# Kernel tuning notes

Hardware: AMD Instinct MI355X
Metric: run time of the kernel (lower is better)

## Reference

```python
import jax, jax.numpy as jnp
import numpy as np

HEADS = 8
DIM_HEAD = 64
EPS = 1e-5

def chan_norm(x, g, b):
    # LayerNorm over channel dim (axis=1), biased variance
    mean = jnp.mean(x, axis=1, keepdims=True)
    var = jnp.var(x, axis=1, keepdims=True)
    return (x - mean) / jnp.sqrt(var + EPS) * g + b

def l2norm(x):
    n = jnp.sqrt(jnp.sum(x * x, axis=1, keepdims=True))
    return x / jnp.maximum(n, 1e-12)

def fold_heads(x, b):
    # b (h c) H W -> (b h) c H W
    _, hc, H, W = x.shape
    return x.reshape(b, HEADS, DIM_HEAD, H, W).reshape(b * HEADS, DIM_HEAD, H, W)

def setup_inputs() -> dict:
    key = jax.random.key(0)
    ks = jax.random.split(key, 8)
    dim = 256
    inner = HEADS * DIM_HEAD  # 512
    b, Hq, Wq = 8, 96, 96
    Hc, Wc = 64, 64
    s = 1.0 / np.sqrt(dim)
    return {
        "query_source": jax.random.normal(ks[0], (b, dim, Hq, Wq), jnp.float32),
        "context": jax.random.normal(ks[1], (b, dim, Hc, Wc), jnp.float32),
        "qs_g": jnp.ones((1, dim, 1, 1), jnp.float32),
        "qs_b": jnp.zeros((1, dim, 1, 1), jnp.float32),
        "ctx_g": jnp.ones((1, dim, 1, 1), jnp.float32),
        "ctx_b": jnp.zeros((1, dim, 1, 1), jnp.float32),
        "out_g": jnp.ones((1, dim, 1, 1), jnp.float32),
        "out_b": jnp.zeros((1, dim, 1, 1), jnp.float32),
        "w_q": jax.random.normal(ks[2], (inner, dim), jnp.float32) * s,
        "w_kv": jax.random.normal(ks[3], (2 * inner, dim), jnp.float32) * s,
        "w_out": jax.random.normal(ks[4], (dim, inner), jnp.float32) * (1.0 / np.sqrt(inner)),
        "gamma": jnp.full((1,), 0.5, jnp.float32),
    }

def reference(query_source, context, qs_g, qs_b, ctx_g, ctx_b, out_g, out_b, w_q, w_kv, w_out, gamma):
    b, c, Hq, Wq = query_source.shape
    Hc, Wc = context.shape[2], context.shape[3]
    h_top_k = int(Hc ** 0.5)
    w_top_k = int(Wc ** 0.5)

    ctx = chan_norm(context, ctx_g, ctx_b)
    qs = chan_norm(query_source, qs_g, qs_b)

    kv = jnp.einsum('oc,bchw->bohw', w_kv, ctx)  # 1x1 conv, no bias
    k, v = jnp.split(kv, 2, axis=1)
    q = jnp.einsum('oc,bchw->bohw', w_q, qs)

    q = fold_heads(q, b); k = fold_heads(k, b); v = fold_heads(v, b)
    q = l2norm(q); k = l2norm(k)  # cosine-sim attention

    if h_top_k < Hc or w_top_k < Wc:
        k_abs = jnp.abs(k)
        q_probe = jnp.sum(q, axis=(2, 3))  # (bh, d)
        if h_top_k < Hc:
            score_r = jnp.einsum('bc,bch->bh', q_probe, jnp.sum(k_abs, axis=3))
            top_h = jax.lax.top_k(score_r, h_top_k)[1]  # (bh, kh)
            k = jnp.take_along_axis(k, top_h[:, None, :, None], axis=2)
            v = jnp.take_along_axis(v, top_h[:, None, :, None], axis=2)
        if w_top_k < Wc:
            score_c = jnp.einsum('bc,bcw->bw', q_probe, jnp.sum(k_abs, axis=2))
            top_w = jax.lax.top_k(score_c, w_top_k)[1]  # (bh, kw)
            k = jnp.take_along_axis(k, top_w[:, None, None, :], axis=3)
            v = jnp.take_along_axis(v, top_w[:, None, None, :], axis=3)

    # b d h w -> b (h w) d
    flat = lambda t: t.transpose(0, 2, 3, 1).reshape(t.shape[0], -1, t.shape[1])
    qf, kf, vf = flat(q), flat(k), flat(v)

    sim = jnp.einsum('bid,bjd->bij', qf, kf)
    attn = jax.nn.softmax(sim, axis=-1)
    out = jnp.einsum('bij,bjd->bid', attn, vf)  # (bh, Hq*Wq, d)

    out = out.reshape(b, HEADS, Hq, Wq, DIM_HEAD).transpose(0, 1, 4, 2, 3)
    out = out.reshape(b, HEADS * DIM_HEAD, Hq, Wq)
    out = jnp.einsum('oc,bchw->bohw', w_out, out)
    out = chan_norm(out, out_g, out_b)
    return gamma * out + query_source
```

## Files before the change

kernel.cpp:

```cpp
#include <hip/hip_runtime.h>
#include <math.h>


#define EPSN 1e-5f

typedef __attribute__((ext_vector_type(8))) short bf16x8;
typedef __attribute__((ext_vector_type(4))) float f32x4;

__device__ inline unsigned short f2bf(float f) {
    unsigned u = __float_as_uint(f);
    u += 0x7fff + ((u >> 16) & 1);
    return (unsigned short)(u >> 16);
}
__device__ inline float bf2f(unsigned short h) {
    return __uint_as_float((unsigned)h << 16);
}

#define GL2LDS(g, s) __builtin_amdgcn_global_load_lds( \
    (const __attribute__((address_space(1))) void*)(g), \
    (__attribute__((address_space(3))) void*)(s), 16, 0, 0)

__global__ __launch_bounds__(256) void cvt_split_kernel(
    const float* __restrict__ x, unsigned short* __restrict__ hi,
    unsigned short* __restrict__ lo, int n)
{
    int i = blockIdx.x * 256 + threadIdx.x;
    if (i < n) {
        float v = x[i];
        unsigned short h = f2bf(v);
        hi[i] = h;
        lo[i] = f2bf(v - bf2f(h));
    }
}
__global__ __launch_bounds__(256) void cvt_bf16_kernel(
    const float* __restrict__ x, unsigned short* __restrict__ y, int n)
{
    int i = blockIdx.x * 256 + threadIdx.x;
    if (i < n) y[i] = f2bf(x[i]);
}

__global__ __launch_bounds__(256) void chan_norm_split_kernel(
    const float* __restrict__ x, const float* __restrict__ g,
    const float* __restrict__ bb, unsigned short* __restrict__ yh,
    unsigned short* __restrict__ yl, int N)
{
    int idx = blockIdx.x * 256 + threadIdx.x;
    int b = idx / N, p = idx - b * N;
    const float* xb = x + (size_t)b * 256 * N + p;
    float mean = 0.f, m2 = 0.f;
    for (int c = 0; c < 256; ++c) {
        float v = xb[(size_t)c * N];
        mean += v; m2 += v * v;
    }
    mean *= (1.f / 256.f); m2 *= (1.f / 256.f);
    float inv = 1.f / sqrtf(m2 - mean * mean + EPSN);
    uint4* yhr = (uint4*)(yh + ((size_t)b * N + p) * 256);
    uint4* ylr = (uint4*)(yl + ((size_t)b * N + p) * 256);
    for (int c0 = 0; c0 < 256; c0 += 8) {
        unsigned short hh[8], ll[8];
        #pragma unroll
        for (int j = 0; j < 8; ++j) {
            int c = c0 + j;
            float v = (xb[(size_t)c * N] - mean) * inv * g[c] + bb[c];
            hh[j] = f2bf(v);
            ll[j] = f2bf(v - bf2f(hh[j]));
        }
        uint4 ph, pl;
        ph.x = (unsigned)hh[0] | ((unsigned)hh[1] << 16);
        ph.y = (unsigned)hh[2] | ((unsigned)hh[3] << 16);
        ph.z = (unsigned)hh[4] | ((unsigned)hh[5] << 16);
        ph.w = (unsigned)hh[6] | ((unsigned)hh[7] << 16);
        pl.x = (unsigned)ll[0] | ((unsigned)ll[1] << 16);
        pl.y = (unsigned)ll[2] | ((unsigned)ll[3] << 16);
        pl.z = (unsigned)ll[4] | ((unsigned)ll[5] << 16);
        pl.w = (unsigned)ll[6] | ((unsigned)ll[7] << 16);
        yhr[c0 >> 3] = ph;
        ylr[c0 >> 3] = pl;
    }
}

template <int MODE>
__global__ __launch_bounds__(256) void gemm_x3(
    const unsigned short* __restrict__ Ah, const unsigned short* __restrict__ Al,
    const unsigned short* __restrict__ Bth, const unsigned short* __restrict__ Btl,
    void* __restrict__ Cv, float* __restrict__ qprobe,
    float* __restrict__ krow, float* __restrict__ kcolp,
    int M, int N, int K, long long strideBt)
{
    __shared__ unsigned short SMEM[4 * 128 * 32];
    unsigned short* AsH = SMEM;
    unsigned short* AsL = SMEM + 4096;
    unsigned short* BsH = SMEM + 8192;
    unsigned short* BsL = SMEM + 12288;
    const unsigned short* BzH = Bth + (size_t)blockIdx.z * strideBt;
    const unsigned short* BzL = Btl + (size_t)blockIdx.z * strideBt;
    int n0 = blockIdx.x * 128, m0 = blockIdx.y * 128;
    int t = threadIdx.x;
    int w = t >> 6, l = t & 63;
    int wm = (w >> 1) * 64, wn = (w & 1) * 64;
    int lc = l & 15, quad = l >> 4;

    f32x4 acc[4][4];
    #pragma unroll
    for (int i = 0; i < 4; ++i)
        #pragma unroll
        for (int j = 0; j < 4; ++j) acc[i][j] = {0.f, 0.f, 0.f, 0.f};

    int srow = t >> 2;
    int sseg = (t & 3) * 8;
    for (int k0 = 0; k0 < K; k0 += 32) {
        size_t a0 = (size_t)(m0 + srow) * K + k0 + sseg;
        size_t a1 = (size_t)(m0 + 64 + srow) * K + k0 + sseg;
        size_t b0 = (size_t)(n0 + srow) * K + k0 + sseg;
        size_t b1 = (size_t)(n0 + 64 + srow) * K + k0 + sseg;
        __syncthreads();
        GL2LDS(Ah + a0, AsH + (size_t)t * 8);
        GL2LDS(Ah + a1, AsH + 2048 + (size_t)t * 8);
        GL2LDS(Al + a0, AsL + (size_t)t * 8);
        GL2LDS(Al + a1, AsL + 2048 + (size_t)t * 8);
        GL2LDS(BzH + b0, BsH + (size_t)t * 8);
        GL2LDS(BzH + b1, BsH + 2048 + (size_t)t * 8);
        GL2LDS(BzL + b0, BsL + (size_t)t * 8);
        GL2LDS(BzL + b1, BsL + 2048 + (size_t)t * 8);
        __syncthreads();
        bf16x8 ah[4], al_[4], bh_[4], bl_[4];
        #pragma unroll
        for (int i = 0; i < 4; ++i) {
            ah[i]  = *(const bf16x8*)(AsH + (size_t)(wm + i * 16 + lc) * 32 + quad * 8);
            al_[i] = *(const bf16x8*)(AsL + (size_t)(wm + i * 16 + lc) * 32 + quad * 8);
        }
        #pragma unroll
        for (int j = 0; j < 4; ++j) {
            bh_[j] = *(const bf16x8*)(BsH + (size_t)(wn + j * 16 + lc) * 32 + quad * 8);
            bl_[j] = *(const bf16x8*)(BsL + (size_t)(wn + j * 16 + lc) * 32 + quad * 8);
        }
        #pragma unroll
        for (int i = 0; i < 4; ++i)
            #pragma unroll
            for (int j = 0; j < 4; ++j) {
                acc[i][j] = __builtin_amdgcn_mfma_f32_16x16x32_bf16(al_[i], bh_[j], acc[i][j], 0, 0, 0);
                acc[i][j] = __builtin_amdgcn_mfma_f32_16x16x32_bf16(ah[i],  bl_[j], acc[i][j], 0, 0, 0);
                acc[i][j] = __builtin_amdgcn_mfma_f32_16x16x32_bf16(ah[i],  bh_[j], acc[i][j], 0, 0, 0);
            }
    }
    float inv[4];
    #pragma unroll
    for (int j = 0; j < 4; ++j) {
        float s = 0.f;
        #pragma unroll
        for (int i = 0; i < 4; ++i)
            #pragma unroll
            for (int r = 0; r < 4; ++r) s += acc[i][j][r] * acc[i][j][r];
        s += __shfl_xor(s, 16);
        s += __shfl_xor(s, 32);
        inv[j] = 1.f / fmaxf(sqrtf(s), 1e-12f);
    }
    unsigned short* qbf = (unsigned short*)Cv;
    #pragma unroll
    for (int i = 0; i < 4; ++i) {
        int row0 = m0 + wm + i * 16 + quad * 4;
        int h = row0 >> 6, d0 = row0 & 63;
        #pragma unroll
        for (int j = 0; j < 4; ++j) {
            int col = n0 + wn + j * 16 + lc;
            size_t addr = ((size_t)(blockIdx.z * 8 + h) * N + col) * 64 + d0;
            unsigned lo = (unsigned)f2bf(acc[i][j][0] * inv[j])
                        | ((unsigned)f2bf(acc[i][j][1] * inv[j]) << 16);
            unsigned hi = (unsigned)f2bf(acc[i][j][2] * inv[j])
                        | ((unsigned)f2bf(acc[i][j][3] * inv[j]) << 16);
            uint2 pk; pk.x = lo; pk.y = hi;
            *(uint2*)(qbf + addr) = pk;
        }
    }
    if (MODE == 1) {
        int bh = blockIdx.z * 8 + ((m0 + wm) >> 6);
        #pragma unroll
        for (int i = 0; i < 4; ++i)
            #pragma unroll
            for (int r = 0; r < 4; ++r) {
                float s = 0.f;
                #pragma unroll
                for (int j = 0; j < 4; ++j) s += acc[i][j][r] * inv[j];
                s += __shfl_xor(s, 1);
                s += __shfl_xor(s, 2);
                s += __shfl_xor(s, 4);
                s += __shfl_xor(s, 8);
                if (lc == 0)
                    atomicAdd(&qprobe[bh * 64 + i * 16 + quad * 4 + r], s);
            }
    }
    if (MODE == 2) {
        int bx = blockIdx.x;
        int th = (n0 + wn) >> 6;
        int headbase = m0 >> 6;
        int hh = w >> 1;
        int bh = blockIdx.z * 8 + headbase + hh;
        #pragma unroll
        for (int i = 0; i < 4; ++i)
            #pragma unroll
            for (int r = 0; r < 4; ++r) {
                float rs = 0.f;
                #pragma unroll
                for (int j = 0; j < 4; ++j) rs += fabsf(acc[i][j][r]) * inv[j];
                rs += __shfl_xor(rs, 1);
                rs += __shfl_xor(rs, 2);
                rs += __shfl_xor(rs, 4);
                rs += __shfl_xor(rs, 8);
                if (lc == 0) {
                    int d = i * 16 + quad * 4 + r;
                    krow[((size_t)bh * 64 + d) * 64 + th] = rs;
                }
            }
        float* colbuf = (float*)SMEM;
        __syncthreads();
        if ((w & 1) == 0) {
            #pragma unroll
            for (int i = 0; i < 4; ++i)
                #pragma unroll
                for (int j = 0; j < 4; ++j)
                    #pragma unroll
                    for (int r = 0; r < 4; ++r)
                        colbuf[(hh * 64 + i * 16 + quad * 4 + r) * 64 + j * 16 + lc]
                            = fabsf(acc[i][j][r]) * inv[j];
        }
        __syncthreads();
        if ((w & 1) == 1) {
            #pragma unroll
            for (int i = 0; i < 4; ++i)
                #pragma unroll
                for (int j = 0; j < 4; ++j)
                    #pragma unroll
                    for (int r = 0; r < 4; ++r)
                        colbuf[(hh * 64 + i * 16 + quad * 4 + r) * 64 + j * 16 + lc]
                            += fabsf(acc[i][j][r]) * inv[j];
        }
        __syncthreads();
        for (int e = t; e < 8192; e += 256) {
            int hh2 = e >> 12, rem = e & 4095;
            int bh2 = blockIdx.z * 8 + headbase + hh2;
            kcolp[((size_t)bh2 * 32 + bx) * 4096 + rem] = colbuf[e];
        }
    }
}

__global__ __launch_bounds__(256) void kcolred_kernel(
    const float* __restrict__ kcolp, float* __restrict__ kcol)
{
    int bh = blockIdx.x;
    int idx = blockIdx.y * 256 + threadIdx.x;
    float s = 0.f;
    #pragma unroll 8
    for (int bx = 0; bx < 32; ++bx)
        s += kcolp[((size_t)bh * 32 + bx) * 4096 + idx];
    kcol[(size_t)bh * 4096 + idx] = s;
}

__global__ __launch_bounds__(256) void gemm_out_fused(
    const unsigned short* __restrict__ A,
    const unsigned short* __restrict__ Bt,
    const float* __restrict__ g, const float* __restrict__ bb,
    const float* __restrict__ gamma, const float* __restrict__ qsrc,
    float* __restrict__ out)
{
    __shared__ unsigned short As[256 * 32];
    __shared__ unsigned short Bs[64 * 32];
    __shared__ float2 colred[4][64];
    int b = blockIdx.z;
    const unsigned short* Bz = Bt + (size_t)b * 9216 * 512;
    int n0 = blockIdx.x * 64;
    int t = threadIdx.x;
    int w = t >> 6, l = t & 63;
    int lc = l & 15, quad = l >> 4;

    f32x4 acc[4][4];
    #pragma unroll
    for (int i = 0; i < 4; ++i)
        #pragma unroll
        for (int j = 0; j < 4; ++j) acc[i][j] = {0.f, 0.f, 0.f, 0.f};

    int srow = t >> 2, sseg = (t & 3) * 8;
    for (int k0 = 0; k0 < 512; k0 += 32) {
        __syncthreads();
        #pragma unroll
        for (int s = 0; s < 4; ++s)
            GL2LDS(A + (size_t)(s * 64 + srow) * 512 + k0 + sseg,
                   As + (size_t)s * 2048 + (size_t)t * 8);
        GL2LDS(Bz + (size_t)(n0 + srow) * 512 + k0 + sseg, Bs + (size_t)t * 8);
        __syncthreads();
        bf16x8 af[4], bfr[4];
        #pragma unroll
        for (int i = 0; i < 4; ++i)
            af[i] = *(const bf16x8*)(As + (size_t)(w * 64 + i * 16 + lc) * 32 + quad * 8);
        #pragma unroll
        for (int j = 0; j < 4; ++j)
            bfr[j] = *(const bf16x8*)(Bs + (size_t)(j * 16 + lc) * 32 + quad * 8);
        #pragma unroll
        for (int i = 0; i < 4; ++i)
            #pragma unroll
            for (int j = 0; j < 4; ++j)
                acc[i][j] = __builtin_amdgcn_mfma_f32_16x16x32_bf16(af[i], bfr[j], acc[i][j], 0, 0, 0);
    }

    float s_[4], ss_[4];
    #pragma unroll
    for (int j = 0; j < 4; ++j) {
        float s = 0.f, ss = 0.f;
        #pragma unroll
        for (int i = 0; i < 4; ++i)
            #pragma unroll
            for (int r = 0; r < 4; ++r) {
                float v = acc[i][j][r];
                s += v; ss += v * v;
            }
        s  += __shfl_xor(s, 16);  s  += __shfl_xor(s, 32);
        ss += __shfl_xor(ss, 16); ss += __shfl_xor(ss, 32);
        s_[j] = s; ss_[j] = ss;
    }
    if (quad == 0) {
        #pragma unroll
        for (int j = 0; j < 4; ++j) {
            colred[w][j * 16 + lc].x = s_[j];
            colred[w][j * 16 + lc].y = ss_[j];
        }
    }
    __syncthreads();
    float mean[4], inv[4];
    #pragma unroll
    for (int j = 0; j < 4; ++j) {
        float ts = 0.f, tss = 0.f;
        #pragma unroll
        for (int ww = 0; ww < 4; ++ww) {
            float2 v = colred[ww][j * 16 + lc];
            ts += v.x; tss += v.y;
        }
        float m = ts * (1.f / 256.f);
        float var = tss * (1.f / 256.f) - m * m;
        mean[j] = m;
        inv[j] = 1.f / sqrtf(var + EPSN);
    }
    float gm = gamma[0];
    const float* qsb = qsrc + (size_t)b * 256 * 9216;
    float* ob = out + (size_t)b * 256 * 9216;
    #pragma unroll
    for (int i = 0; i < 4; ++i)
        #pragma unroll
        for (int r = 0; r < 4; ++r) {
            int row = w * 64 + i * 16 + quad * 4 + r;
            float gg = g[row], bv = bb[row];
            #pragma unroll
            for (int j = 0; j < 4; ++j) {
                int col = n0 + j * 16 + lc;
                float v = (acc[i][j][r] - mean[j]) * inv[j] * gg + bv;
                ob[(size_t)row * 9216 + col] = gm * v + qsb[(size_t)row * 9216 + col];
            }
        }
}

__global__ void topk_kernel(const float* __restrict__ qprobe,
                            const float* __restrict__ krow,
                            const float* __restrict__ kcol,
                            int* __restrict__ toph, int* __restrict__ topw)
{
    int bh = blockIdx.x, t = threadIdx.x;
    __shared__ float qp[64], sr[64], sc[64];
    qp[t] = qprobe[bh * 64 + t];
    __syncthreads();
    float s1 = 0.f, s2 = 0.f;
    for (int d = 0; d < 64; ++d) {
        float qv = qp[d];
        s1 += qv * krow[((size_t)bh * 64 + d) * 64 + t];
        s2 += qv * kcol[((size_t)bh * 64 + d) * 64 + t];
    }
    sr[t] = s1; sc[t] = s2;
    __syncthreads();
    if (t == 0) {
        unsigned long long used = 0ull;
        for (int it = 0; it < 8; ++it) {
            int best = -1; float bv = -INFINITY;
            for (int i = 0; i < 64; ++i)
                if (!((used >> i) & 1ull) && sr[i] > bv) { bv = sr[i]; best = i; }
            if (best < 0) best = it;
            used |= 1ull << best;
            toph[bh * 8 + it] = best;
        }
        used = 0ull;
        for (int it = 0; it < 8; ++it) {
            int best = -1; float bv = -INFINITY;
            for (int i = 0; i < 64; ++i)
                if (!((used >> i) & 1ull) && sc[i] > bv) { bv = sc[i]; best = i; }
            if (best < 0) best = it;
            used |= 1ull << best;
            topw[bh * 8 + it] = best;
        }
    }
}

__global__ __launch_bounds__(256) void gather_k_kernel(
    const unsigned short* __restrict__ kn,
    const int* __restrict__ toph, const int* __restrict__ topw,
    unsigned short* __restrict__ ksel)
{
    int bh = blockIdx.x;
    __shared__ int th_s[8], tw_s[8];
    if (threadIdx.x < 8) th_s[threadIdx.x] = toph[bh * 8 + threadIdx.x];
    else if (threadIdx.x < 16) tw_s[threadIdx.x - 8] = topw[bh * 8 + threadIdx.x - 8];
    __syncthreads();
    int tok = threadIdx.x >> 2, sg = threadIdx.x & 3;
    int p = th_s[tok >> 3] * 64 + tw_s[tok & 7];
    const uint4* src = (const uint4*)(kn + ((size_t)bh * 4096 + p) * 64 + sg * 16);
    uint4* dst = (uint4*)(ksel + ((size_t)bh * 64 + tok) * 64 + sg * 16);
    dst[0] = src[0];
    dst[1] = src[1];
}

__global__ __launch_bounds__(256) void vsel_kernel(
    const float* __restrict__ w_kv, const unsigned short* __restrict__ ctxt,
    const int* __restrict__ toph, const int* __restrict__ topw,
    unsigned short* __restrict__ vt)
{
    int bh = blockIdx.x, b = bh >> 3, h = bh & 7;
    __shared__ int th_s[8], tw_s[8];
    if (threadIdx.x < 8) th_s[threadIdx.x] = toph[bh * 8 + threadIdx.x];
    else if (threadIdx.x < 16) tw_s[threadIdx.x - 8] = topw[bh * 8 + threadIdx.x - 8];
    __syncthreads();
    const unsigned short* cb = ctxt + (size_t)b * 4096 * 256;
    int l = blockIdx.y * 1024 + threadIdx.x;
    for (int it = 0; it < 4; ++it, l += 256) {
        int tok = l >> 6, d = l & 63;
        int p = th_s[tok >> 3] * 64 + tw_s[tok & 7];
        const float* wr = w_kv + (size_t)(512 + h * 64 + d) * 256;
        const unsigned short* cr = cb + (size_t)p * 256;
        float s = 0.f;
        for (int c = 0; c < 256; ++c) s += wr[c] * bf2f(cr[c]);
        vt[(size_t)bh * 4096 + d * 64 + tok] = f2bf(s);
    }
}

#define LPAD 72
__global__ __launch_bounds__(256) void attn_mfma_kernel(
    const unsigned short* __restrict__ q_pd, const unsigned short* __restrict__ ksel,
    const unsigned short* __restrict__ vt, unsigned short* __restrict__ attn_t)
{
    int bh = blockIdx.y, b = bh >> 3, h = bh & 7;
    __shared__ unsigned short Ks[64 * LPAD];
    __shared__ unsigned short Vs[64 * LPAD];
    __shared__ unsigned short Ps[4][16 * LPAD];
    int t = threadIdx.x, w = t >> 6, l = t & 63;
    int lc = l & 15, quad = l >> 4;
    {
        int r0 = t >> 3, c0 = (t & 7) * 8;
        const unsigned short* kg = ksel + (size_t)bh * 4096;
        const unsigned short* vg = vt + (size_t)bh * 4096;
        *(uint4*)(Ks + r0 * LPAD + c0)        = *(const uint4*)(kg + r0 * 64 + c0);
        *(uint4*)(Ks + (r0 + 32) * LPAD + c0) = *(const uint4*)(kg + (r0 + 32) * 64 + c0);
        *(uint4*)(Vs + r0 * LPAD + c0)        = *(const uint4*)(vg + r0 * 64 + c0);
        *(uint4*)(Vs + (r0 + 32) * LPAD + c0) = *(const uint4*)(vg + (r0 + 32) * 64 + c0);
    }
    __syncthreads();
    int p0 = blockIdx.x * 64 + w * 16;
    const unsigned short* qrow = q_pd + ((size_t)bh * 9216 + p0 + lc) * 64;
    bf16x8 aq0 = *(const bf16x8*)(qrow + quad * 8);
    bf16x8 aq1 = *(const bf16x8*)(qrow + 32 + quad * 8);
    f32x4 sacc[4];
    #pragma unroll
    for (int j = 0; j < 4; ++j) sacc[j] = {0.f, 0.f, 0.f, 0.f};
    #pragma unroll
    for (int j = 0; j < 4; ++j) {
        bf16x8 bk0 = *(const bf16x8*)(Ks + (j * 16 + lc) * LPAD + quad * 8);
        bf16x8 bk1 = *(const bf16x8*)(Ks + (j * 16 + lc) * LPAD + 32 + quad * 8);
        sacc[j] = __builtin_amdgcn_mfma_f32_16x16x32_bf16(aq0, bk0, sacc[j], 0, 0, 0);
        sacc[j] = __builtin_amdgcn_mfma_f32_16x16x32_bf16(aq1, bk1, sacc[j], 0, 0, 0);
    }
    float e[4][4], den[4] = {0.f, 0.f, 0.f, 0.f};
    #pragma unroll
    for (int j = 0; j < 4; ++j)
        #pragma unroll
        for (int r = 0; r < 4; ++r) {
            float v = __expf(sacc[j][r] - 1.f);
            e[j][r] = v; den[r] += v;
        }
    #pragma unroll
    for (int r = 0; r < 4; ++r) {
        den[r] += __shfl_xor(den[r], 1);
        den[r] += __shfl_xor(den[r], 2);
        den[r] += __shfl_xor(den[r], 4);
        den[r] += __shfl_xor(den[r], 8);
    }
    #pragma unroll
    for (int j = 0; j < 4; ++j)
        #pragma unroll
        for (int r = 0; r < 4; ++r)
            Ps[w][(quad * 4 + r) * LPAD + j * 16 + lc] = f2bf(e[j][r]);
    __syncthreads();
    bf16x8 ap0 = *(const bf16x8*)(Ps[w] + lc * LPAD + quad * 8);
    bf16x8 ap1 = *(const bf16x8*)(Ps[w] + lc * LPAD + 32 + quad * 8);
    f32x4 oacc[4];
    #pragma unroll
    for (int j = 0; j < 4; ++j) oacc[j] = {0.f, 0.f, 0.f, 0.f};
    #pragma unroll
    for (int j = 0; j < 4; ++j) {
        bf16x8 bv0 = *(const bf16x8*)(Vs + (j * 16 + lc) * LPAD + quad * 8);
        bf16x8 bv1 = *(const bf16x8*)(Vs + (j * 16 + lc) * LPAD + 32 + quad * 8);
        oacc[j] = __builtin_amdgcn_mfma_f32_16x16x32_bf16(ap0, bv0, oacc[j], 0, 0, 0);
        oacc[j] = __builtin_amdgcn_mfma_f32_16x16x32_bf16(ap1, bv1, oacc[j], 0, 0, 0);
    }
    float rd[4];
    #pragma unroll
    for (int r = 0; r < 4; ++r) rd[r] = 1.f / den[r];
    #pragma unroll
    for (int j = 0; j < 4; ++j)
        #pragma unroll
        for (int r = 0; r < 4; ++r) {
            int p = p0 + quad * 4 + r;
            int d = j * 16 + lc;
            attn_t[((size_t)b * 9216 + p) * 512 + h * 64 + d] = f2bf(oacc[j][r] * rd[r]);
        }
}

extern "C" void kernel_launch(void* const* d_in, const int* in_sizes, int n_in,
                              void* d_out, int out_size, void* d_ws, size_t ws_size,
                              hipStream_t stream) {
    const float* qsrc  = (const float*)d_in[0];
    const float* ctx   = (const float*)d_in[1];
    const float* qs_g  = (const float*)d_in[2];
    const float* qs_b  = (const float*)d_in[3];
    const float* ctx_g = (const float*)d_in[4];
    const float* ctx_b = (const float*)d_in[5];
    const float* out_g = (const float*)d_in[6];
    const float* out_b = (const float*)d_in[7];
    const float* w_q   = (const float*)d_in[8];
    const float* w_kv  = (const float*)d_in[9];
    const float* w_out = (const float*)d_in[10];
    const float* gamma = (const float*)d_in[11];
    float* out = (float*)d_out;

    char* base = (char*)d_ws;
    unsigned short* qs_h  = (unsigned short*)(base + 0);
    unsigned short* qs_l  = (unsigned short*)(base + 37748736);
    unsigned short* kn    = (unsigned short*)(base + 0);
    float*          kcolp = (float*)        (base + 33554432);
    float*          krow  = (float*)        (base + 67108864);
    float*          kcol  = (float*)        (base + 68157440);
    unsigned short* attn_t= (unsigned short*)(base + 0);
    unsigned short* q_pd  = (unsigned short*)(base + 75497472);
    unsigned short* ctx_h = (unsigned short*)(base + 150994944);
    unsigned short* ctx_l = (unsigned short*)(base + 167772160);
    char* S = base + 184549376;
    float* qprob = (float*)S;                     S += 4096 * 4;
    unsigned short* ksel = (unsigned short*)S;    S += 262144 * 2;
    unsigned short* vt   = (unsigned short*)S;    S += 262144 * 2;
    int*   toph  = (int*)S;                       S += 512 * 4;
    int*   topw  = (int*)S;                       S += 512 * 4;
    unsigned short* wq_h = (unsigned short*)S;    S += 131072 * 2;
    unsigned short* wq_l = (unsigned short*)S;    S += 131072 * 2;
    unsigned short* wk_h = (unsigned short*)S;    S += 131072 * 2;
    unsigned short* wk_l = (unsigned short*)S;    S += 131072 * 2;
    unsigned short* wo_h = (unsigned short*)S;    S += 131072 * 2;

    cvt_split_kernel<<<512, 256, 0, stream>>>(w_q, wq_h, wq_l, 131072);
    cvt_split_kernel<<<512, 256, 0, stream>>>(w_kv, wk_h, wk_l, 131072);
    cvt_bf16_kernel<<<512, 256, 0, stream>>>(w_out, wo_h, 131072);
    hipMemsetAsync(qprob, 0, 4096 * sizeof(float), stream);
    chan_norm_split_kernel<<<288, 256, 0, stream>>>(qsrc, qs_g, qs_b, qs_h, qs_l, 9216);
    gemm_x3<1><<<dim3(72, 4, 8), 256, 0, stream>>>(
        wq_h, wq_l, qs_h, qs_l, q_pd, qprob, nullptr, nullptr,
        512, 9216, 256, 9216LL * 256);
    chan_norm_split_kernel<<<128, 256, 0, stream>>>(ctx, ctx_g, ctx_b, ctx_h, ctx_l, 4096);
    gemm_x3<2><<<dim3(32, 4, 8), 256, 0, stream>>>(
        wk_h, wk_l, ctx_h, ctx_l, kn, nullptr, krow, kcolp,
        512, 4096, 256, 4096LL * 256);
    kcolred_kernel<<<dim3(64, 16), 256, 0, stream>>>(kcolp, kcol);
    topk_kernel<<<64, 64, 0, stream>>>(qprob, krow, kcol, toph, topw);
    gather_k_kernel<<<64, 256, 0, stream>>>(kn, toph, topw, ksel);
    vsel_kernel<<<dim3(64, 4), 256, 0, stream>>>(w_kv, ctx_h, toph, topw, vt);
    attn_mfma_kernel<<<dim3(144, 64), 256, 0, stream>>>(q_pd, ksel, vt, attn_t);
    gemm_out_fused<<<dim3(144, 1, 8), 256, 0, stream>>>(
        wo_h, attn_t, out_g, out_b, gamma, qsrc, out);
}
```

Measured before the change: 694.1 us.

## Fuse attention and output projection with channel norm into one kernel

Merges the per-head attention kernel and the output GEMM+chan_norm kernel. Each block now loops over all 8 heads for a 64-position tile, keeps the per-head attention output in LDS, and accumulates the w_out projection directly in registers. This removes the bf16 attn_t round-trip through global memory and one kernel launch. In exchange there are fewer, longer blocks (1152 vs 9216), more LDS per block, and w_out is read straight from global memory per head.

```diff
diff --git a/kernel.cpp b/kernel.cpp
--- a/kernel.cpp
+++ b/kernel.cpp
@@ -253,107 +253,6 @@
     for (int bx = 0; bx < 32; ++bx)
         s += kcolp[((size_t)bh * 32 + bx) * 4096 + idx];
     kcol[(size_t)bh * 4096 + idx] = s;
-}
-
-__global__ __launch_bounds__(256) void gemm_out_fused(
-    const unsigned short* __restrict__ A,
-    const unsigned short* __restrict__ Bt,
-    const float* __restrict__ g, const float* __restrict__ bb,
-    const float* __restrict__ gamma, const float* __restrict__ qsrc,
-    float* __restrict__ out)
-{
-    __shared__ unsigned short As[256 * 32];
-    __shared__ unsigned short Bs[64 * 32];
-    __shared__ float2 colred[4][64];
-    int b = blockIdx.z;
-    const unsigned short* Bz = Bt + (size_t)b * 9216 * 512;
-    int n0 = blockIdx.x * 64;
-    int t = threadIdx.x;
-    int w = t >> 6, l = t & 63;
-    int lc = l & 15, quad = l >> 4;
-
-    f32x4 acc[4][4];
-    #pragma unroll
-    for (int i = 0; i < 4; ++i)
-        #pragma unroll
-        for (int j = 0; j < 4; ++j) acc[i][j] = {0.f, 0.f, 0.f, 0.f};
-
-    int srow = t >> 2, sseg = (t & 3) * 8;
-    for (int k0 = 0; k0 < 512; k0 += 32) {
-        __syncthreads();
-        #pragma unroll
-        for (int s = 0; s < 4; ++s)
-            GL2LDS(A + (size_t)(s * 64 + srow) * 512 + k0 + sseg,
-                   As + (size_t)s * 2048 + (size_t)t * 8);
-        GL2LDS(Bz + (size_t)(n0 + srow) * 512 + k0 + sseg, Bs + (size_t)t * 8);
-        __syncthreads();
-        bf16x8 af[4], bfr[4];
-        #pragma unroll
-        for (int i = 0; i < 4; ++i)
-            af[i] = *(const bf16x8*)(As + (size_t)(w * 64 + i * 16 + lc) * 32 + quad * 8);
-        #pragma unroll
-        for (int j = 0; j < 4; ++j)
-            bfr[j] = *(const bf16x8*)(Bs + (size_t)(j * 16 + lc) * 32 + quad * 8);
-        #pragma unroll
-        for (int i = 0; i < 4; ++i)
-            #pragma unroll
-            for (int j = 0; j < 4; ++j)
-                acc[i][j] = __builtin_amdgcn_mfma_f32_16x16x32_bf16(af[i], bfr[j], acc[i][j], 0, 0, 0);
-    }
-
-    float s_[4], ss_[4];
-    #pragma unroll
-    for (int j = 0; j < 4; ++j) {
-        float s = 0.f, ss = 0.f;
-        #pragma unroll
-        for (int i = 0; i < 4; ++i)
-            #pragma unroll
-            for (int r = 0; r < 4; ++r) {
-                float v = acc[i][j][r];
-                s += v; ss += v * v;
-            }
-        s  += __shfl_xor(s, 16);  s  += __shfl_xor(s, 32);
-        ss += __shfl_xor(ss, 16); ss += __shfl_xor(ss, 32);
-        s_[j] = s; ss_[j] = ss;
-    }
-    if (quad == 0) {
-        #pragma unroll
-        for (int j = 0; j < 4; ++j) {
-            colred[w][j * 16 + lc].x = s_[j];
-            colred[w][j * 16 + lc].y = ss_[j];
-        }
-    }
-    __syncthreads();
-    float mean[4], inv[4];
-    #pragma unroll
-    for (int j = 0; j < 4; ++j) {
-        float ts = 0.f, tss = 0.f;
-        #pragma unroll
-        for (int ww = 0; ww < 4; ++ww) {
-            float2 v = colred[ww][j * 16 + lc];
-            ts += v.x; tss += v.y;
-        }
-        float m = ts * (1.f / 256.f);
-        float var = tss * (1.f / 256.f) - m * m;
-        mean[j] = m;
-        inv[j] = 1.f / sqrtf(var + EPSN);
-    }
-    float gm = gamma[0];
-    const float* qsb = qsrc + (size_t)b * 256 * 9216;
-    float* ob = out + (size_t)b * 256 * 9216;
-    #pragma unroll
-    for (int i = 0; i < 4; ++i)
-        #pragma unroll
-        for (int r = 0; r < 4; ++r) {
-            int row = w * 64 + i * 16 + quad * 4 + r;
-            float gg = g[row], bv = bb[row];
-            #pragma unroll
-            for (int j = 0; j < 4; ++j) {
-                int col = n0 + j * 16 + lc;
-                float v = (acc[i][j][r] - mean[j]) * inv[j] * gg + bv;
-                ob[(size_t)row * 9216 + col] = gm * v + qsb[(size_t)row * 9216 + col];
-            }
-        }
 }
 
 __global__ void topk_kernel(const float* __restrict__ qprobe,
@@ -437,83 +336,169 @@
 }
 
 #define LPAD 72
-__global__ __launch_bounds__(256) void attn_mfma_kernel(
+__global__ __launch_bounds__(256) void attn_out_fused(
     const unsigned short* __restrict__ q_pd, const unsigned short* __restrict__ ksel,
-    const unsigned short* __restrict__ vt, unsigned short* __restrict__ attn_t)
-{
-    int bh = blockIdx.y, b = bh >> 3, h = bh & 7;
+    const unsigned short* __restrict__ vt, const unsigned short* __restrict__ wo,
+    const float* __restrict__ g, const float* __restrict__ bb,
+    const float* __restrict__ gamma, const float* __restrict__ qsrc,
+    float* __restrict__ out)
+{
+    int b = blockIdx.y;
+    int p0 = blockIdx.x * 64;
     __shared__ unsigned short Ks[64 * LPAD];
     __shared__ unsigned short Vs[64 * LPAD];
-    __shared__ unsigned short Ps[4][16 * LPAD];
+    __shared__ unsigned short Ph[4][16 * LPAD];
+    __shared__ unsigned short Ahs[64 * LPAD];
+    __shared__ float2 colred[4][64];
     int t = threadIdx.x, w = t >> 6, l = t & 63;
     int lc = l & 15, quad = l >> 4;
-    {
-        int r0 = t >> 3, c0 = (t & 7) * 8;
-        const unsigned short* kg = ksel + (size_t)bh * 4096;
-        const unsigned short* vg = vt + (size_t)bh * 4096;
-        *(uint4*)(Ks + r0 * LPAD + c0)        = *(const uint4*)(kg + r0 * 64 + c0);
-        *(uint4*)(Ks + (r0 + 32) * LPAD + c0) = *(const uint4*)(kg + (r0 + 32) * 64 + c0);
-        *(uint4*)(Vs + r0 * LPAD + c0)        = *(const uint4*)(vg + r0 * 64 + c0);
-        *(uint4*)(Vs + (r0 + 32) * LPAD + c0) = *(const uint4*)(vg + (r0 + 32) * 64 + c0);
+
+    f32x4 pacc[4][4];
+    #pragma unroll
+    for (int i = 0; i < 4; ++i)
+        #pragma unroll
+        for (int j = 0; j < 4; ++j) pacc[i][j] = {0.f, 0.f, 0.f, 0.f};
+
+    for (int h = 0; h < 8; ++h) {
+        int bh = b * 8 + h;
+        __syncthreads();
+        {
+            int r0 = t >> 3, c0 = (t & 7) * 8;
+            const unsigned short* kg = ksel + (size_t)bh * 4096;
+            const unsigned short* vg = vt + (size_t)bh * 4096;
+            *(uint4*)(Ks + r0 * LPAD + c0)        = *(const uint4*)(kg + r0 * 64 + c0);
+            *(uint4*)(Ks + (r0 + 32) * LPAD + c0) = *(const uint4*)(kg + (r0 + 32) * 64 + c0);
+            *(uint4*)(Vs + r0 * LPAD + c0)        = *(const uint4*)(vg + r0 * 64 + c0);
+            *(uint4*)(Vs + (r0 + 32) * LPAD + c0) = *(const uint4*)(vg + (r0 + 32) * 64 + c0);
+        }
+        __syncthreads();
+        const unsigned short* qrow = q_pd + ((size_t)bh * 9216 + p0 + w * 16 + lc) * 64;
+        bf16x8 aq0 = *(const bf16x8*)(qrow + quad * 8);
+        bf16x8 aq1 = *(const bf16x8*)(qrow + 32 + quad * 8);
+        f32x4 sacc[4];
+        #pragma unroll
+        for (int j = 0; j < 4; ++j) sacc[j] = {0.f, 0.f, 0.f, 0.f};
+        #pragma unroll
+        for (int j = 0; j < 4; ++j) {
+            bf16x8 bk0 = *(const bf16x8*)(Ks + (j * 16 + lc) * LPAD + quad * 8);
+            bf16x8 bk1 = *(const bf16x8*)(Ks + (j * 16 + lc) * LPAD + 32 + quad * 8);
+            sacc[j] = __builtin_amdgcn_mfma_f32_16x16x32_bf16(aq0, bk0, sacc[j], 0, 0, 0);
+            sacc[j] = __builtin_amdgcn_mfma_f32_16x16x32_bf16(aq1, bk1, sacc[j], 0, 0, 0);
+        }
+        float e[4][4], den[4] = {0.f, 0.f, 0.f, 0.f};
+        #pragma unroll
+        for (int j = 0; j < 4; ++j)
+            #pragma unroll
+            for (int r = 0; r < 4; ++r) {
+                float v = __expf(sacc[j][r] - 1.f);
+                e[j][r] = v; den[r] += v;
+            }
+        #pragma unroll
+        for (int r = 0; r < 4; ++r) {
+            den[r] += __shfl_xor(den[r], 1);
+            den[r] += __shfl_xor(den[r], 2);
+            den[r] += __shfl_xor(den[r], 4);
+            den[r] += __shfl_xor(den[r], 8);
+        }
+        #pragma unroll
+        for (int j = 0; j < 4; ++j)
+            #pragma unroll
+            for (int r = 0; r < 4; ++r)
+                Ph[w][(quad * 4 + r) * LPAD + j * 16 + lc] = f2bf(e[j][r]);
+        __syncthreads();
+        bf16x8 ap0 = *(const bf16x8*)(Ph[w] + lc * LPAD + quad * 8);
+        bf16x8 ap1 = *(const bf16x8*)(Ph[w] + lc * LPAD + 32 + quad * 8);
+        f32x4 oacc[4];
+        #pragma unroll
+        for (int j = 0; j < 4; ++j) oacc[j] = {0.f, 0.f, 0.f, 0.f};
+        #pragma unroll
+        for (int j = 0; j < 4; ++j) {
+            bf16x8 bv0 = *(const bf16x8*)(Vs + (j * 16 + lc) * LPAD + quad * 8);
+            bf16x8 bv1 = *(const bf16x8*)(Vs + (j * 16 + lc) * LPAD + 32 + quad * 8);
+            oacc[j] = __builtin_amdgcn_mfma_f32_16x16x32_bf16(ap0, bv0, oacc[j], 0, 0, 0);
+            oacc[j] = __builtin_amdgcn_mfma_f32_16x16x32_bf16(ap1, bv1, oacc[j], 0, 0, 0);
+        }
+        float rd[4];
+        #pragma unroll
+        for (int r = 0; r < 4; ++r) rd[r] = 1.f / den[r];
+        #pragma unroll
+        for (int j = 0; j < 4; ++j)
+            #pragma unroll
+            for (int r = 0; r < 4; ++r)
+                Ahs[(w * 16 + quad * 4 + r) * LPAD + j * 16 + lc] = f2bf(oacc[j][r] * rd[r]);
+        __syncthreads();
+        #pragma unroll
+        for (int k0 = 0; k0 < 64; k0 += 32) {
+            bf16x8 af[4], bfr[4];
+            #pragma unroll
+            for (int i = 0; i < 4; ++i) {
+                int row = w * 64 + i * 16 + lc;
+                af[i] = *(const bf16x8*)(wo + (size_t)row * 512 + h * 64 + k0 + quad * 8);
+            }
+            #pragma unroll
+            for (int j = 0; j < 4; ++j)
+                bfr[j] = *(const bf16x8*)(Ahs + (size_t)(j * 16 + lc) * LPAD + k0 + quad * 8);
+            #pragma unroll
+            for (int i = 0; i < 4; ++i)
+                #pragma unroll
+                for (int j = 0; j < 4; ++j)
+                    pacc[i][j] = __builtin_amdgcn_mfma_f32_16x16x32_bf16(af[i], bfr[j], pacc[i][j], 0, 0, 0);
+        }
+    }
+
+    float s_[4], ss_[4];
+    #pragma unroll
+    for (int j = 0; j < 4; ++j) {
+        float s = 0.f, ss = 0.f;
+        #pragma unroll
+        for (int i = 0; i < 4; ++i)
+            #pragma unroll
+            for (int r = 0; r < 4; ++r) {
+                float v = pacc[i][j][r];
+                s += v; ss += v * v;
+            }
+        s  += __shfl_xor(s, 16);  s  += __shfl_xor(s, 32);
+        ss += __shfl_xor(ss, 16); ss += __shfl_xor(ss, 32);
+        s_[j] = s; ss_[j] = ss;
     }
     __syncthreads();
-    int p0 = blockIdx.x * 64 + w * 16;
-    const unsigned short* qrow = q_pd + ((size_t)bh * 9216 + p0 + lc) * 64;
-    bf16x8 aq0 = *(const bf16x8*)(qrow + quad * 8);
-    bf16x8 aq1 = *(const bf16x8*)(qrow + 32 + quad * 8);
-    f32x4 sacc[4];
-    #pragma unroll
-    for (int j = 0; j < 4; ++j) sacc[j] = {0.f, 0.f, 0.f, 0.f};
+    if (quad == 0) {
+        #pragma unroll
+        for (int j = 0; j < 4; ++j) {
+            colred[w][j * 16 + lc].x = s_[j];
+            colred[w][j * 16 + lc].y = ss_[j];
+        }
+    }
+    __syncthreads();
+    float mean[4], inv[4];
     #pragma unroll
     for (int j = 0; j < 4; ++j) {
-        bf16x8 bk0 = *(const bf16x8*)(Ks + (j * 16 + lc) * LPAD + quad * 8);
-        bf16x8 bk1 = *(const bf16x8*)(Ks + (j * 16 + lc) * LPAD + 32 + quad * 8);
-        sacc[j] = __builtin_amdgcn_mfma_f32_16x16x32_bf16(aq0, bk0, sacc[j], 0, 0, 0);
-        sacc[j] = __builtin_amdgcn_mfma_f32_16x16x32_bf16(aq1, bk1, sacc[j], 0, 0, 0);
-    }
-    float e[4][4], den[4] = {0.f, 0.f, 0.f, 0.f};
-    #pragma unroll
-    for (int j = 0; j < 4; ++j)
+        float ts = 0.f, tss = 0.f;
+        #pragma unroll
+        for (int ww = 0; ww < 4; ++ww) {
+            float2 v = colred[ww][j * 16 + lc];
+            ts += v.x; tss += v.y;
+        }
+        float m = ts * (1.f / 256.f);
+        float var = tss * (1.f / 256.f) - m * m;
+        mean[j] = m;
+        inv[j] = 1.f / sqrtf(var + EPSN);
+    }
+    float gm = gamma[0];
+    const float* qsb = qsrc + (size_t)b * 256 * 9216;
+    float* ob = out + (size_t)b * 256 * 9216;
+    #pragma unroll
+    for (int i = 0; i < 4; ++i)
         #pragma unroll
         for (int r = 0; r < 4; ++r) {
-            float v = __expf(sacc[j][r] - 1.f);
-            e[j][r] = v; den[r] += v;
-        }
-    #pragma unroll
-    for (int r = 0; r < 4; ++r) {
-        den[r] += __shfl_xor(den[r], 1);
-        den[r] += __shfl_xor(den[r], 2);
-        den[r] += __shfl_xor(den[r], 4);
-        den[r] += __shfl_xor(den[r], 8);
-    }
-    #pragma unroll
-    for (int j = 0; j < 4; ++j)
-        #pragma unroll
-        for (int r = 0; r < 4; ++r)
-            Ps[w][(quad * 4 + r) * LPAD + j * 16 + lc] = f2bf(e[j][r]);
-    __syncthreads();
-    bf16x8 ap0 = *(const bf16x8*)(Ps[w] + lc * LPAD + quad * 8);
-    bf16x8 ap1 = *(const bf16x8*)(Ps[w] + lc * LPAD + 32 + quad * 8);
-    f32x4 oacc[4];
-    #pragma unroll
-    for (int j = 0; j < 4; ++j) oacc[j] = {0.f, 0.f, 0.f, 0.f};
-    #pragma unroll
-    for (int j = 0; j < 4; ++j) {
-        bf16x8 bv0 = *(const bf16x8*)(Vs + (j * 16 + lc) * LPAD + quad * 8);
-        bf16x8 bv1 = *(const bf16x8*)(Vs + (j * 16 + lc) * LPAD + 32 + quad * 8);
-        oacc[j] = __builtin_amdgcn_mfma_f32_16x16x32_bf16(ap0, bv0, oacc[j], 0, 0, 0);
-        oacc[j] = __builtin_amdgcn_mfma_f32_16x16x32_bf16(ap1, bv1, oacc[j], 0, 0, 0);
-    }
-    float rd[4];
-    #pragma unroll
-    for (int r = 0; r < 4; ++r) rd[r] = 1.f / den[r];
-    #pragma unroll
-    for (int j = 0; j < 4; ++j)
-        #pragma unroll
-        for (int r = 0; r < 4; ++r) {
-            int p = p0 + quad * 4 + r;
-            int d = j * 16 + lc;
-            attn_t[((size_t)b * 9216 + p) * 512 + h * 64 + d] = f2bf(oacc[j][r] * rd[r]);
+            int row = w * 64 + i * 16 + quad * 4 + r;
+            float gg = g[row], bv = bb[row];
+            #pragma unroll
+            for (int j = 0; j < 4; ++j) {
+                int col = p0 + j * 16 + lc;
+                float v = (pacc[i][j][r] - mean[j]) * inv[j] * gg + bv;
+                ob[(size_t)row * 9216 + col] = gm * v + qsb[(size_t)row * 9216 + col];
+            }
         }
 }
 
@@ -541,7 +526,6 @@
     float*          kcolp = (float*)        (base + 33554432);
     float*          krow  = (float*)        (base + 67108864);
     float*          kcol  = (float*)        (base + 68157440);
-    unsigned short* attn_t= (unsigned short*)(base + 0);
     unsigned short* q_pd  = (unsigned short*)(base + 75497472);
     unsigned short* ctx_h = (unsigned short*)(base + 150994944);
     unsigned short* ctx_l = (unsigned short*)(base + 167772160);
@@ -573,7 +557,6 @@
     topk_kernel<<<64, 64, 0, stream>>>(qprob, krow, kcol, toph, topw);
     gather_k_kernel<<<64, 256, 0, stream>>>(kn, toph, topw, ksel);
     vsel_kernel<<<dim3(64, 4), 256, 0, stream>>>(w_kv, ctx_h, toph, topw, vt);
-    attn_mfma_kernel<<<dim3(144, 64), 256, 0, stream>>>(q_pd, ksel, vt, attn_t);
-    gemm_out_fused<<<dim3(144, 1, 8), 256, 0, stream>>>(
-        wo_h, attn_t, out_g, out_b, gamma, qsrc, out);
-}
+    attn_out_fused<<<dim3(144, 8), 256, 0, stream>>>(
+        q_pd, ksel, vt, wo_h, out_g, out_b, gamma, qsrc, out);
+}
```

New measurement: 699.4 us. Within noise of the previous version (+0.8%).
